# Kernel tuning notes

Hardware: AMD Instinct MI355X
Metric: run time of the kernel (lower is better)

Reference implementation:

```python
import jax, jax.numpy as jnp
import numpy as np

DIM = 64
HEADS = 8
SR = 8
HEAD_DIM = DIM // HEADS
SCALE = HEAD_DIM ** -0.5


def layernorm(x, g, b, eps=1e-5):
    mu = jnp.mean(x, axis=-1, keepdims=True)
    var = jnp.var(x, axis=-1, keepdims=True)
    return (x - mu) * jax.lax.rsqrt(var + eps) * g + b


def setup_inputs() -> dict:
    key = jax.random.key(0)
    ks = jax.random.split(key, 6)
    B, Hh, Ww = 2, 128, 128
    N = Hh * Ww
    s = 0.02
    return {
        "x": jax.random.normal(ks[0], (B, N, DIM), jnp.float32),
        "H": Hh,
        "W": Ww,
        "q_w": jax.random.normal(ks[1], (DIM, DIM), jnp.float32) * s,
        "kv_w": jax.random.normal(ks[2], (DIM, 2 * DIM), jnp.float32) * s,
        "sr_w": jax.random.normal(ks[3], (DIM, DIM, SR, SR), jnp.float32) * s,
        "sr_b": jnp.zeros((DIM,), jnp.float32),
        "ln_g": jnp.ones((DIM,), jnp.float32),
        "ln_b": jnp.zeros((DIM,), jnp.float32),
        "proj_w": jax.random.normal(ks[4], (DIM, DIM), jnp.float32) * s,
        "proj_b": jnp.zeros((DIM,), jnp.float32),
    }


def reference(x, q_w, kv_w, sr_w, sr_b, ln_g, ln_b, proj_w, proj_b, H, W):
    B, N, C = x.shape
    # queries: [B, heads, N, head_dim]
    q = (x @ q_w).reshape(B, N, HEADS, HEAD_DIM).transpose(0, 2, 1, 3)
    # spatial reduction of KV tokens: conv stride=kernel=SR over the HxW grid
    x_ = x.transpose(0, 2, 1).reshape(B, C, H, W)
    x_ = jax.lax.conv_general_dilated(
        x_, sr_w, window_strides=(SR, SR), padding="VALID",
        dimension_numbers=("NCHW", "OIHW", "NCHW"),
    ) + sr_b[None, :, None, None]
    x_ = x_.reshape(B, C, -1).transpose(0, 2, 1)  # [B, Nk, C], Nk = (H/SR)*(W/SR)
    x_ = layernorm(x_, ln_g, ln_b)
    kv = (x_ @ kv_w).reshape(B, -1, 2, HEADS, HEAD_DIM)
    k = kv[:, :, 0].transpose(0, 2, 1, 3)  # [B, heads, Nk, hd]
    v = kv[:, :, 1].transpose(0, 2, 1, 3)
    attn = jax.nn.softmax(jnp.einsum("bhnd,bhmd->bhnm", q, k) * SCALE, axis=-1)
    out = jnp.einsum("bhnm,bhmd->bhnd", attn, v).transpose(0, 2, 1, 3).reshape(B, N, C)
    return out @ proj_w + proj_b
```

## Files before the change

### kernel.cpp

```cpp
#include <hip/hip_runtime.h>
#include <math.h>

#define NB 2
#define NTOK 16384
#define CDIM 64
#define WIMG 128
#define NKV 256
#define NHEAD 8
#define HDIM 8
#define RTOKS 512
#define NSLICE 32

typedef unsigned short u16;
typedef __attribute__((ext_vector_type(8))) short bf16x8;
typedef __attribute__((ext_vector_type(4))) unsigned int u32x4;
typedef __attribute__((ext_vector_type(2))) unsigned int u32x2;
typedef __attribute__((ext_vector_type(16))) float f32x16;

constexpr float KSCALE = 0.35355339059327373f * 1.4426950408889634f;

__device__ __forceinline__ u16 f2bf(float f) {
  unsigned u = __builtin_bit_cast(unsigned, f);
  return (u16)((u + 0x7FFFu + ((u >> 16) & 1u)) >> 16);
}
__device__ __forceinline__ float bf2f(u16 h) {
  return __builtin_bit_cast(float, (unsigned)h << 16);
}

__device__ __forceinline__ f32x16 mfma32x16(bf16x8 a, bf16x8 b, f32x16 c) {
  return __builtin_amdgcn_mfma_f32_32x32x16_bf16(a, b, c, 0, 0, 0);
}

__device__ __forceinline__ void pl32swap(unsigned &a, unsigned &b) {
  u32x2 r = __builtin_amdgcn_permlane32_swap(a, b, false, false);
  a = r[0]; b = r[1];
}

__device__ __forceinline__ float fexp2(float x) {
  float r;
  asm("v_exp_f32 %0, %1" : "=v"(r) : "v"(x));
  return r;
}

__device__ __forceinline__ void split8(const float* v, bf16x8& hout, bf16x8& lout) {
  unsigned hw[4], lw[4];
  float hf[8], lof[8];
  #pragma unroll
  for (int q = 0; q < 4; ++q)
    asm("v_cvt_pk_bf16_f32 %0, %1, %2" : "=v"(hw[q]) : "v"(v[2*q]), "v"(v[2*q+1]));
  #pragma unroll
  for (int q = 0; q < 4; ++q) {
    hf[2*q]   = __builtin_bit_cast(float, hw[q] << 16);
    hf[2*q+1] = __builtin_bit_cast(float, hw[q] & 0xFFFF0000u);
  }
  #pragma unroll
  for (int j = 0; j < 8; ++j) lof[j] = v[j] - hf[j];
  #pragma unroll
  for (int q = 0; q < 4; ++q)
    asm("v_cvt_pk_bf16_f32 %0, %1, %2" : "=v"(lw[q]) : "v"(lof[2*q]), "v"(lof[2*q+1]));
  u32x4 H; H[0] = hw[0]; H[1] = hw[1]; H[2] = hw[2]; H[3] = hw[3];
  u32x4 L; L[0] = lw[0]; L[1] = lw[1]; L[2] = lw[2]; L[3] = lw[3];
  hout = __builtin_bit_cast(bf16x8, H);
  lout = __builtin_bit_cast(bf16x8, L);
}

__device__ __forceinline__ float wave_reduce_sum64(float v) {
  #pragma unroll
  for (int off = 32; off > 0; off >>= 1) v += __shfl_xor(v, off, 64);
  return v;
}

__global__ __launch_bounds__(256) void k0_pack(const float* __restrict__ srw,
                                               const float* __restrict__ qw,
                                               const float* __restrict__ pw,
                                               u16* __restrict__ wpk_hi, u16* __restrict__ wpk_lo,
                                               u16* __restrict__ qpk_hi, u16* __restrict__ qpk_lo,
                                               u16* __restrict__ ppk_hi, u16* __restrict__ ppk_lo) {
  int idx = blockIdx.x * 256 + threadIdx.x;
  if (idx < 262144) {
    const int j   = idx & 7;
    const int oc  = (idx >> 3) & 63;
    const int hi  = (idx >> 9) & 1;
    const int icg = (idx >> 10) & 3;
    const int s   = idx >> 12;
    const float v = srw[oc * 4096 + (icg * 16 + hi * 8 + j) * 64 + s];
    const u16 h = f2bf(v);
    wpk_hi[idx] = h;
    wpk_lo[idx] = f2bf(v - bf2f(h));
  } else if (idx < 262144 + 4096) {
    const int q = idx - 262144;
    const int j   = q & 7;
    const int o   = (q >> 3) & 63;
    const int hi  = (q >> 9) & 1;
    const int icg = q >> 10;
    const float v = qw[(icg * 16 + hi * 8 + j) * 64 + o];
    const u16 h = f2bf(v);
    qpk_hi[q] = h;
    qpk_lo[q] = f2bf(v - bf2f(h));
  } else if (idx < 262144 + 8192) {
    const int q = idx - 262144 - 4096;
    const int j  = q & 7;
    const int o  = (q >> 3) & 63;
    const int hi = (q >> 9) & 1;
    const int g  = q >> 10;
    const float v = pw[(g * 16 + hi * 8 + j) * 64 + o];
    const u16 h = f2bf(v);
    ppk_hi[q] = h;
    ppk_lo[q] = f2bf(v - bf2f(h));
  }
}

__global__ __launch_bounds__(256) void kAQ_conv_qproj(const float* __restrict__ x,
                                                      const u16* __restrict__ wpk_hi,
                                                      const u16* __restrict__ wpk_lo,
                                                      const u16* __restrict__ qpk_hi,
                                                      const u16* __restrict__ qpk_lo,
                                                      float* __restrict__ pbuf,
                                                      u16* __restrict__ qbuf) {
  const int t = threadIdx.x;
  const int lane = t & 63;
  const int lo = lane & 31;
  const int hi = lane >> 5;
  const int w = t >> 6;
  const int oc0 = (w & 1) * 32;
  const int blk = blockIdx.x;

  if (blk < 256) {
    const int th = w >> 1;
    const int tile = blk & 15;
    const int kc = blk >> 4;
    const int tg = tile * 32 + lo;
    const int b = tg >> 8;
    const int p = tg & 255;

    f32x16 c;
    #pragma unroll
    for (int i = 0; i < 16; ++i) c[i] = 0.f;

    #pragma unroll
    for (int sp = 0; sp < 2; ++sp) {
      const int s = kc * 4 + th * 2 + sp;
      const int kh = s >> 3, kw = s & 7;
      const int nrow = ((p >> 4) * 8 + kh) * WIMG + (p & 15) * 8 + kw;
      const float* xr = x + ((size_t)b * NTOK + nrow) * CDIM;
      #pragma unroll
      for (int icg = 0; icg < 4; ++icg) {
        const int ic0 = icg * 16 + hi * 8;
        float4 a0 = *(const float4*)(xr + ic0);
        float4 a1 = *(const float4*)(xr + ic0 + 4);
        float v[8] = {a0.x, a0.y, a0.z, a0.w, a1.x, a1.y, a1.z, a1.w};
        bf16x8 ah, al;
        split8(v, ah, al);
        const size_t widx = ((((size_t)s * 4 + icg) * 2 + hi) * 64 + (oc0 + lo)) * 8;
        bf16x8 bh = *(const bf16x8*)(wpk_hi + widx);
        bf16x8 bl = *(const bf16x8*)(wpk_lo + widx);
        c = mfma32x16(ah, bh, c);
        c = mfma32x16(ah, bl, c);
        c = mfma32x16(al, bh, c);
      }
    }
    const int slice = kc * 2 + th;
    #pragma unroll
    for (int r = 0; r < 16; ++r) {
      const int tokr = (r & 3) + 8 * (r >> 2) + 4 * hi;
      pbuf[((size_t)slice * RTOKS + tile * 32 + tokr) * 64 + oc0 + lo] = c[r];
    }
  } else {
    const int qblk = blk - 256;
    const int b = qblk >> 8;
    const int tok0 = ((qblk & 255) * 2 + (w >> 1)) * 32;

    f32x16 c;
    #pragma unroll
    for (int i = 0; i < 16; ++i) c[i] = 0.f;

    const float* xr = x + ((size_t)b * NTOK + tok0 + lo) * CDIM;
    #pragma unroll
    for (int icg = 0; icg < 4; ++icg) {
      const int ic0 = icg * 16 + hi * 8;
      float4 a0 = *(const float4*)(xr + ic0);
      float4 a1 = *(const float4*)(xr + ic0 + 4);
      float v[8] = {a0.x, a0.y, a0.z, a0.w, a1.x, a1.y, a1.z, a1.w};
      bf16x8 ah, al;
      split8(v, ah, al);
      const size_t qidx = (((size_t)icg * 2 + hi) * 64 + (oc0 + lo)) * 8;
      bf16x8 bh = *(const bf16x8*)(qpk_hi + qidx);
      bf16x8 bl = *(const bf16x8*)(qpk_lo + qidx);
      c = mfma32x16(ah, bh, c);
      c = mfma32x16(ah, bl, c);
      c = mfma32x16(al, bh, c);
    }
    const int oc = oc0 + lo;
    const int h = oc >> 3, d = oc & 7;
    u16* qb = qbuf + (((size_t)b * NHEAD + h) * NTOK) * HDIM + d;
    #pragma unroll
    for (int r = 0; r < 16; ++r) {
      const int tok = tok0 + (r & 3) + 8 * (r >> 2) + 4 * hi;
      qb[(size_t)tok * HDIM] = f2bf(c[r]);
    }
  }
}

__global__ __launch_bounds__(256) void k2_ln_kv(const float* __restrict__ pbuf,
                                                const float* __restrict__ srb,
                                                const float* __restrict__ lng,
                                                const float* __restrict__ lnb,
                                                const float* __restrict__ kvw,
                                                u16* __restrict__ kbuf,
                                                u16* __restrict__ vbufT) {
  __shared__ float ylds[4][64];
  const int t = threadIdx.x;
  const int wv = t >> 6;
  const int o  = t & 63;
  const int tg = blockIdx.x * 4 + wv;
  float y = srb[o];
  #pragma unroll 8
  for (int s = 0; s < NSLICE; ++s) y += pbuf[((size_t)s * RTOKS + tg) * 64 + o];
  const float sum   = wave_reduce_sum64(y);
  const float sumsq = wave_reduce_sum64(y * y);
  const float mu  = sum * (1.f / 64.f);
  const float var = sumsq * (1.f / 64.f) - mu * mu;
  const float rstd = rsqrtf(var + 1e-5f);
  const float yn = (y - mu) * rstd * lng[o] + lnb[o];
  ylds[wv][o] = yn;
  __syncthreads();
  float ka = 0.f, va = 0.f;
  #pragma unroll 16
  for (int i = 0; i < 64; ++i) {
    const float yv = ylds[wv][i];
    ka += yv * kvw[i * 128 + o];
    va += yv * kvw[i * 128 + 64 + o];
  }
  const int b = tg >> 8, pp = tg & 255;
  const int h = o >> 3, d = o & 7;
  const int bh = b * NHEAD + h;
  kbuf[((size_t)bh * NKV + pp) * HDIM + d] = f2bf(ka * KSCALE);
  vbufT[((size_t)bh * HDIM + d) * NKV + pp] = f2bf(va);
}

__global__ __launch_bounds__(256) void k4_attn_mfma(const u16* __restrict__ qbuf,
                                                    const u16* __restrict__ kbuf,
                                                    const u16* __restrict__ vbufT,
                                                    float* __restrict__ abuf) {
  const int t = threadIdx.x;
  const int lane = t & 63;
  const int w = blockIdx.x * 4 + (t >> 6);
  const int bh = w >> 7;
  const int wi = w & 127;
  const int lo = lane & 31;
  const int hi = lane >> 5;

  bf16x8 kf[8];
  const u16* kb = kbuf + (size_t)bh * NKV * HDIM;
  #pragma unroll
  for (int c = 0; c < 8; ++c) {
    bf16x8 z = {0, 0, 0, 0, 0, 0, 0, 0};
    if (hi == 0) z = *(const bf16x8*)(kb + (c * 32 + lo) * HDIM);
    kf[c] = z;
  }

  const short one_bf = (short)0x3F80;
  bf16x8 vf[16];
  const u16* vb = vbufT + (size_t)bh * HDIM * NKV;
  #pragma unroll
  for (int f = 0; f < 16; ++f) {
    bf16x8 z = {0, 0, 0, 0, 0, 0, 0, 0};
    if (lo < 8) {
      z = *(const bf16x8*)(vb + lo * NKV + f * 16 + hi * 8);
    } else if (lo == 8) {
      bf16x8 o1 = {one_bf, one_bf, one_bf, one_bf, one_bf, one_bf, one_bf, one_bf};
      z = o1;
    }
    vf[f] = z;
  }

  #pragma unroll
  for (int cp = 0; cp < 2; ++cp) {
    const int qtA = (wi * 4 + cp * 2) * 32;
    const int qtB = qtA + 32;
    bf16x8 qfA = {0, 0, 0, 0, 0, 0, 0, 0};
    bf16x8 qfB = {0, 0, 0, 0, 0, 0, 0, 0};
    if (hi == 0) {
      qfA = *(const bf16x8*)(qbuf + ((size_t)bh * NTOK + qtA + lo) * HDIM);
      qfB = *(const bf16x8*)(qbuf + ((size_t)bh * NTOK + qtB + lo) * HDIM);
    }

    f32x16 oA, oB;
    #pragma unroll
    for (int i = 0; i < 16; ++i) { oA[i] = 0.f; oB[i] = 0.f; }

    #pragma unroll
    for (int kblk = 0; kblk < 8; ++kblk) {
      f32x16 sA, sB;
      #pragma unroll
      for (int i = 0; i < 16; ++i) { sA[i] = 0.f; sB[i] = 0.f; }
      sA = mfma32x16(kf[kblk], qfA, sA);
      sB = mfma32x16(kf[kblk], qfB, sB);

      #pragma unroll
      for (int r = 0; r < 16; ++r) sA[r] = fexp2(sA[r]);
      #pragma unroll
      for (int r = 0; r < 16; ++r) sB[r] = fexp2(sB[r]);

      unsigned pkA01[4], pkA23[4], pkB01[4], pkB23[4];
      #pragma unroll
      for (int q = 0; q < 4; ++q) {
        asm("v_cvt_pk_bf16_f32 %0, %1, %2" : "=v"(pkA01[q]) : "v"(sA[4*q+0]), "v"(sA[4*q+1]));
        asm("v_cvt_pk_bf16_f32 %0, %1, %2" : "=v"(pkA23[q]) : "v"(sA[4*q+2]), "v"(sA[4*q+3]));
      }
      #pragma unroll
      for (int q = 0; q < 4; ++q) {
        asm("v_cvt_pk_bf16_f32 %0, %1, %2" : "=v"(pkB01[q]) : "v"(sB[4*q+0]), "v"(sB[4*q+1]));
        asm("v_cvt_pk_bf16_f32 %0, %1, %2" : "=v"(pkB23[q]) : "v"(sB[4*q+2]), "v"(sB[4*q+3]));
      }
      #pragma unroll
      for (int jj = 0; jj < 2; ++jj) {
        unsigned a0 = pkA01[2*jj], b0 = pkA01[2*jj+1];
        unsigned a1 = pkA23[2*jj], b1 = pkA23[2*jj+1];
        pl32swap(a0, b0);
        pl32swap(a1, b1);
        u32x4 wv; wv[0] = a0; wv[1] = a1; wv[2] = b0; wv[3] = b1;
        bf16x8 pfrag = __builtin_bit_cast(bf16x8, wv);
        oA = mfma32x16(vf[kblk * 2 + jj], pfrag, oA);
      }
      #pragma unroll
      for (int jj = 0; jj < 2; ++jj) {
        unsigned a0 = pkB01[2*jj], b0 = pkB01[2*jj+1];
        unsigned a1 = pkB23[2*jj], b1 = pkB23[2*jj+1];
        pl32swap(a0, b0);
        pl32swap(a1, b1);
        u32x4 wv; wv[0] = a0; wv[1] = a1; wv[2] = b0; wv[3] = b1;
        bf16x8 pfrag = __builtin_bit_cast(bf16x8, wv);
        oB = mfma32x16(vf[kblk * 2 + jj], pfrag, oB);
      }
    }

    {
      float d0 = oA[4];
      float d1 = __shfl_xor(d0, 32, 64);
      const float den = hi ? d1 : d0;
      const float r = 1.0f / den;
      float4 o;
      o.x = oA[0] * r; o.y = oA[1] * r; o.z = oA[2] * r; o.w = oA[3] * r;
      *(float4*)(abuf + ((size_t)bh * NTOK + qtA + lo) * HDIM + hi * 4) = o;
    }
    {
      float d0 = oB[4];
      float d1 = __shfl_xor(d0, 32, 64);
      const float den = hi ? d1 : d0;
      const float r = 1.0f / den;
      float4 o;
      o.x = oB[0] * r; o.y = oB[1] * r; o.z = oB[2] * r; o.w = oB[3] * r;
      *(float4*)(abuf + ((size_t)bh * NTOK + qtB + lo) * HDIM + hi * 4) = o;
    }
  }
}

__global__ __launch_bounds__(256) void kP_proj(const float* __restrict__ abuf,
                                               const u16* __restrict__ ppk_hi,
                                               const u16* __restrict__ ppk_lo,
                                               const float* __restrict__ pb,
                                               float* __restrict__ out) {
  const int t = threadIdx.x;
  const int lane = t & 63;
  const int lo = lane & 31;
  const int hi = lane >> 5;
  const int w = t >> 6;
  const int oc0 = (w & 1) * 32;
  const int blk = blockIdx.x;
  const int b = blk >> 8;
  const int tok0 = ((blk & 255) * 2 + (w >> 1)) * 32;

  f32x16 c;
  #pragma unroll
  for (int i = 0; i < 16; ++i) c[i] = 0.f;

  #pragma unroll
  for (int f = 0; f < 4; ++f) {
    const int h = 2 * f + hi;
    const float* src = abuf + (((size_t)b * NHEAD + h) * NTOK + tok0 + lo) * HDIM;
    float4 a0 = *(const float4*)(src);
    float4 a1 = *(const float4*)(src + 4);
    float v[8] = {a0.x, a0.y, a0.z, a0.w, a1.x, a1.y, a1.z, a1.w};
    bf16x8 ah, al;
    split8(v, ah, al);
    const size_t pidx = (((size_t)f * 2 + hi) * 64 + (oc0 + lo)) * 8;
    bf16x8 bh = *(const bf16x8*)(ppk_hi + pidx);
    bf16x8 bl = *(const bf16x8*)(ppk_lo + pidx);
    c = mfma32x16(ah, bh, c);
    c = mfma32x16(ah, bl, c);
    c = mfma32x16(al, bh, c);
  }
  const float pbv = pb[oc0 + lo];
  #pragma unroll
  for (int r = 0; r < 16; ++r) {
    const int tok = tok0 + (r & 3) + 8 * (r >> 2) + 4 * hi;
    out[((size_t)b * NTOK + tok) * CDIM + oc0 + lo] = c[r] + pbv;
  }
}

extern "C" void kernel_launch(void* const* d_in, const int* in_sizes, int n_in,
                              void* d_out, int out_size, void* d_ws, size_t ws_size,
                              hipStream_t stream) {
  const float* x    = (const float*)d_in[0];
  const float* qw   = (const float*)d_in[3];
  const float* kvw  = (const float*)d_in[4];
  const float* srw  = (const float*)d_in[5];
  const float* srb  = (const float*)d_in[6];
  const float* lng  = (const float*)d_in[7];
  const float* lnb  = (const float*)d_in[8];
  const float* pw   = (const float*)d_in[9];
  const float* pb   = (const float*)d_in[10];
  float* out = (float*)d_out;
  char* base = (char*)d_ws;

  u16*   wpk_hi = (u16*)(base);
  u16*   wpk_lo = (u16*)(base + 524288);
  u16*   qpk_hi = (u16*)(base + 1048576);
  u16*   qpk_lo = (u16*)(base + 1056768);
  u16*   ppk_hi = (u16*)(base + 1064960);
  u16*   ppk_lo = (u16*)(base + 1073152);
  float* pbuf   = (float*)(base + 1081344);
  u16*   kbuf   = (u16*)(base + 5275648);
  u16*   vbufT  = (u16*)(base + 5341184);
  u16*   qbuf   = (u16*)(base + 5406720);
  float* abuf   = (float*)(base + 9601024);

  k0_pack<<<1056, 256, 0, stream>>>(srw, qw, pw, wpk_hi, wpk_lo,
                                    qpk_hi, qpk_lo, ppk_hi, ppk_lo);
  kAQ_conv_qproj<<<768, 256, 0, stream>>>(x, wpk_hi, wpk_lo, qpk_hi, qpk_lo,
                                          pbuf, qbuf);
  k2_ln_kv<<<128, 256, 0, stream>>>(pbuf, srb, lng, lnb, kvw, kbuf, vbufT);
  k4_attn_mfma<<<512, 256, 0, stream>>>(qbuf, kbuf, vbufT, abuf);
  kP_proj<<<512, 256, 0, stream>>>(abuf, ppk_hi, ppk_lo, pb, out);
}
```

Measured before the change: 42.01 us.

## Halve per-wave attention work and stream V fragments with software prefetch

The attention kernel now gives each wave 64 query tokens instead of 128 and launches twice as many blocks. It no longer preloads all 16 V fragments into registers; it loads two per key block and prefetches the next block's pair. The intent is to cut register pressure, raise occupancy and parallelism, and hide V load latency. In exchange, K fragments are loaded twice as often in total, and the per-iteration V loads add global traffic inside the loop.

```diff
diff --git a/kernel.cpp b/kernel.cpp
--- a/kernel.cpp
+++ b/kernel.cpp
@@ -245,13 +245,15 @@
   const int t = threadIdx.x;
   const int lane = t & 63;
   const int w = blockIdx.x * 4 + (t >> 6);
-  const int bh = w >> 7;
-  const int wi = w & 127;
+  const int bh = w >> 8;
+  const int wi = w & 255;
   const int lo = lane & 31;
   const int hi = lane >> 5;
 
+  const u16* kb = kbuf + (size_t)bh * NKV * HDIM;
+  const u16* vb = vbufT + (size_t)bh * HDIM * NKV;
+
   bf16x8 kf[8];
-  const u16* kb = kbuf + (size_t)bh * NKV * HDIM;
   #pragma unroll
   for (int c = 0; c < 8; ++c) {
     bf16x8 z = {0, 0, 0, 0, 0, 0, 0, 0};
@@ -259,100 +261,115 @@
     kf[c] = z;
   }
 
+  const int qtA = (wi * 2) * 32;
+  const int qtB = qtA + 32;
+  bf16x8 qfA = {0, 0, 0, 0, 0, 0, 0, 0};
+  bf16x8 qfB = {0, 0, 0, 0, 0, 0, 0, 0};
+  if (hi == 0) {
+    qfA = *(const bf16x8*)(qbuf + ((size_t)bh * NTOK + qtA + lo) * HDIM);
+    qfB = *(const bf16x8*)(qbuf + ((size_t)bh * NTOK + qtB + lo) * HDIM);
+  }
+
+  f32x16 oA, oB;
+  #pragma unroll
+  for (int i = 0; i < 16; ++i) { oA[i] = 0.f; oB[i] = 0.f; }
+
   const short one_bf = (short)0x3F80;
-  bf16x8 vf[16];
-  const u16* vb = vbufT + (size_t)bh * HDIM * NKV;
-  #pragma unroll
-  for (int f = 0; f < 16; ++f) {
-    bf16x8 z = {0, 0, 0, 0, 0, 0, 0, 0};
-    if (lo < 8) {
-      z = *(const bf16x8*)(vb + lo * NKV + f * 16 + hi * 8);
-    } else if (lo == 8) {
-      bf16x8 o1 = {one_bf, one_bf, one_bf, one_bf, one_bf, one_bf, one_bf, one_bf};
-      z = o1;
-    }
-    vf[f] = z;
-  }
-
-  #pragma unroll
-  for (int cp = 0; cp < 2; ++cp) {
-    const int qtA = (wi * 4 + cp * 2) * 32;
-    const int qtB = qtA + 32;
-    bf16x8 qfA = {0, 0, 0, 0, 0, 0, 0, 0};
-    bf16x8 qfB = {0, 0, 0, 0, 0, 0, 0, 0};
-    if (hi == 0) {
-      qfA = *(const bf16x8*)(qbuf + ((size_t)bh * NTOK + qtA + lo) * HDIM);
-      qfB = *(const bf16x8*)(qbuf + ((size_t)bh * NTOK + qtB + lo) * HDIM);
-    }
-
-    f32x16 oA, oB;
-    #pragma unroll
-    for (int i = 0; i < 16; ++i) { oA[i] = 0.f; oB[i] = 0.f; }
-
-    #pragma unroll
-    for (int kblk = 0; kblk < 8; ++kblk) {
-      f32x16 sA, sB;
-      #pragma unroll
-      for (int i = 0; i < 16; ++i) { sA[i] = 0.f; sB[i] = 0.f; }
-      sA = mfma32x16(kf[kblk], qfA, sA);
-      sB = mfma32x16(kf[kblk], qfB, sB);
-
-      #pragma unroll
-      for (int r = 0; r < 16; ++r) sA[r] = fexp2(sA[r]);
-      #pragma unroll
-      for (int r = 0; r < 16; ++r) sB[r] = fexp2(sB[r]);
-
-      unsigned pkA01[4], pkA23[4], pkB01[4], pkB23[4];
-      #pragma unroll
-      for (int q = 0; q < 4; ++q) {
-        asm("v_cvt_pk_bf16_f32 %0, %1, %2" : "=v"(pkA01[q]) : "v"(sA[4*q+0]), "v"(sA[4*q+1]));
-        asm("v_cvt_pk_bf16_f32 %0, %1, %2" : "=v"(pkA23[q]) : "v"(sA[4*q+2]), "v"(sA[4*q+3]));
-      }
-      #pragma unroll
-      for (int q = 0; q < 4; ++q) {
-        asm("v_cvt_pk_bf16_f32 %0, %1, %2" : "=v"(pkB01[q]) : "v"(sB[4*q+0]), "v"(sB[4*q+1]));
-        asm("v_cvt_pk_bf16_f32 %0, %1, %2" : "=v"(pkB23[q]) : "v"(sB[4*q+2]), "v"(sB[4*q+3]));
-      }
-      #pragma unroll
-      for (int jj = 0; jj < 2; ++jj) {
-        unsigned a0 = pkA01[2*jj], b0 = pkA01[2*jj+1];
-        unsigned a1 = pkA23[2*jj], b1 = pkA23[2*jj+1];
-        pl32swap(a0, b0);
-        pl32swap(a1, b1);
-        u32x4 wv; wv[0] = a0; wv[1] = a1; wv[2] = b0; wv[3] = b1;
-        bf16x8 pfrag = __builtin_bit_cast(bf16x8, wv);
-        oA = mfma32x16(vf[kblk * 2 + jj], pfrag, oA);
-      }
-      #pragma unroll
-      for (int jj = 0; jj < 2; ++jj) {
-        unsigned a0 = pkB01[2*jj], b0 = pkB01[2*jj+1];
-        unsigned a1 = pkB23[2*jj], b1 = pkB23[2*jj+1];
-        pl32swap(a0, b0);
-        pl32swap(a1, b1);
-        u32x4 wv; wv[0] = a0; wv[1] = a1; wv[2] = b0; wv[3] = b1;
-        bf16x8 pfrag = __builtin_bit_cast(bf16x8, wv);
-        oB = mfma32x16(vf[kblk * 2 + jj], pfrag, oB);
-      }
-    }
-
+  const bf16x8 vzero = {0, 0, 0, 0, 0, 0, 0, 0};
+  const bf16x8 vones = {one_bf, one_bf, one_bf, one_bf, one_bf, one_bf, one_bf, one_bf};
+  bf16x8 vf0n = (lo == 8) ? vones : vzero;
+  bf16x8 vf1n = vf0n;
+  if (lo < 8) {
+    vf0n = *(const bf16x8*)(vb + lo * NKV + 0 + hi * 8);
+    vf1n = *(const bf16x8*)(vb + lo * NKV + 16 + hi * 8);
+  }
+
+  #pragma unroll
+  for (int kblk = 0; kblk < 8; ++kblk) {
+    const bf16x8 vf0 = vf0n;
+    const bf16x8 vf1 = vf1n;
+    if (kblk < 7 && lo < 8) {
+      vf0n = *(const bf16x8*)(vb + lo * NKV + (kblk + 1) * 32 + hi * 8);
+      vf1n = *(const bf16x8*)(vb + lo * NKV + (kblk + 1) * 32 + 16 + hi * 8);
+    }
+
+    f32x16 sA, sB;
+    #pragma unroll
+    for (int i = 0; i < 16; ++i) { sA[i] = 0.f; sB[i] = 0.f; }
+    sA = mfma32x16(kf[kblk], qfA, sA);
+    sB = mfma32x16(kf[kblk], qfB, sB);
+
+    #pragma unroll
+    for (int r = 0; r < 16; ++r) sA[r] = fexp2(sA[r]);
+    #pragma unroll
+    for (int r = 0; r < 16; ++r) sB[r] = fexp2(sB[r]);
+
+    unsigned pkA01[4], pkA23[4], pkB01[4], pkB23[4];
+    #pragma unroll
+    for (int q = 0; q < 4; ++q) {
+      asm("v_cvt_pk_bf16_f32 %0, %1, %2" : "=v"(pkA01[q]) : "v"(sA[4*q+0]), "v"(sA[4*q+1]));
+      asm("v_cvt_pk_bf16_f32 %0, %1, %2" : "=v"(pkA23[q]) : "v"(sA[4*q+2]), "v"(sA[4*q+3]));
+    }
+    #pragma unroll
+    for (int q = 0; q < 4; ++q) {
+      asm("v_cvt_pk_bf16_f32 %0, %1, %2" : "=v"(pkB01[q]) : "v"(sB[4*q+0]), "v"(sB[4*q+1]));
+      asm("v_cvt_pk_bf16_f32 %0, %1, %2" : "=v"(pkB23[q]) : "v"(sB[4*q+2]), "v"(sB[4*q+3]));
+    }
     {
-      float d0 = oA[4];
-      float d1 = __shfl_xor(d0, 32, 64);
-      const float den = hi ? d1 : d0;
-      const float r = 1.0f / den;
-      float4 o;
-      o.x = oA[0] * r; o.y = oA[1] * r; o.z = oA[2] * r; o.w = oA[3] * r;
-      *(float4*)(abuf + ((size_t)bh * NTOK + qtA + lo) * HDIM + hi * 4) = o;
+      unsigned a0 = pkA01[0], b0 = pkA01[1];
+      unsigned a1 = pkA23[0], b1 = pkA23[1];
+      pl32swap(a0, b0);
+      pl32swap(a1, b1);
+      u32x4 wv; wv[0] = a0; wv[1] = a1; wv[2] = b0; wv[3] = b1;
+      bf16x8 pfrag = __builtin_bit_cast(bf16x8, wv);
+      oA = mfma32x16(vf0, pfrag, oA);
     }
     {
-      float d0 = oB[4];
-      float d1 = __shfl_xor(d0, 32, 64);
-      const float den = hi ? d1 : d0;
-      const float r = 1.0f / den;
-      float4 o;
-      o.x = oB[0] * r; o.y = oB[1] * r; o.z = oB[2] * r; o.w = oB[3] * r;
-      *(float4*)(abuf + ((size_t)bh * NTOK + qtB + lo) * HDIM + hi * 4) = o;
-    }
+      unsigned a0 = pkA01[2], b0 = pkA01[3];
+      unsigned a1 = pkA23[2], b1 = pkA23[3];
+      pl32swap(a0, b0);
+      pl32swap(a1, b1);
+      u32x4 wv; wv[0] = a0; wv[1] = a1; wv[2] = b0; wv[3] = b1;
+      bf16x8 pfrag = __builtin_bit_cast(bf16x8, wv);
+      oA = mfma32x16(vf1, pfrag, oA);
+    }
+    {
+      unsigned a0 = pkB01[0], b0 = pkB01[1];
+      unsigned a1 = pkB23[0], b1 = pkB23[1];
+      pl32swap(a0, b0);
+      pl32swap(a1, b1);
+      u32x4 wv; wv[0] = a0; wv[1] = a1; wv[2] = b0; wv[3] = b1;
+      bf16x8 pfrag = __builtin_bit_cast(bf16x8, wv);
+      oB = mfma32x16(vf0, pfrag, oB);
+    }
+    {
+      unsigned a0 = pkB01[2], b0 = pkB01[3];
+      unsigned a1 = pkB23[2], b1 = pkB23[3];
+      pl32swap(a0, b0);
+      pl32swap(a1, b1);
+      u32x4 wv; wv[0] = a0; wv[1] = a1; wv[2] = b0; wv[3] = b1;
+      bf16x8 pfrag = __builtin_bit_cast(bf16x8, wv);
+      oB = mfma32x16(vf1, pfrag, oB);
+    }
+  }
+
+  {
+    float d0 = oA[4];
+    float d1 = __shfl_xor(d0, 32, 64);
+    const float den = hi ? d1 : d0;
+    const float r = 1.0f / den;
+    float4 o;
+    o.x = oA[0] * r; o.y = oA[1] * r; o.z = oA[2] * r; o.w = oA[3] * r;
+    *(float4*)(abuf + ((size_t)bh * NTOK + qtA + lo) * HDIM + hi * 4) = o;
+  }
+  {
+    float d0 = oB[4];
+    float d1 = __shfl_xor(d0, 32, 64);
+    const float den = hi ? d1 : d0;
+    const float r = 1.0f / den;
+    float4 o;
+    o.x = oB[0] * r; o.y = oB[1] * r; o.z = oB[2] * r; o.w = oB[3] * r;
+    *(float4*)(abuf + ((size_t)bh * NTOK + qtB + lo) * HDIM + hi * 4) = o;
   }
 }
 
@@ -431,6 +448,6 @@
   kAQ_conv_qproj<<<768, 256, 0, stream>>>(x, wpk_hi, wpk_lo, qpk_hi, qpk_lo,
                                           pbuf, qbuf);
   k2_ln_kv<<<128, 256, 0, stream>>>(pbuf, srb, lng, lnb, kvw, kbuf, vbufT);
-  k4_attn_mfma<<<512, 256, 0, stream>>>(qbuf, kbuf, vbufT, abuf);
+  k4_attn_mfma<<<1024, 256, 0, stream>>>(qbuf, kbuf, vbufT, abuf);
   kP_proj<<<512, 256, 0, stream>>>(abuf, ppk_hi, ppk_lo, pb, out);
 }
```

New measurement: 41.50 us, median of 2. No clear change (-1.2%).
